# Optimization experiments

Hardware: AMD Instinct MI355X
Metric: run time of the kernel (lower is better)

The kernel has to match this reference:

```python
import jax, jax.numpy as jnp
import numpy as np
import math

B, L, DM = 2, 256, 256
H, NK, T = 8, 4, 4  # heads, num_kernels, time_dim
DH = DM // H


def _gauss_mean_over_d(t, mu, sigma, w):
    """t: [B,P,T]; mu/sigma/w: [H,D,T,K] -> mean over D of sum_{t,k} w*exp(...): [B,H,P].
    Scans over D to avoid materializing [B,H,D,P,T,K]."""
    D = mu.shape[1]

    def step(acc, p):
        mu_d, sg_d, w_d = p  # each [H,T,K]
        diff = t[:, None, :, :, None] - mu_d[None, :, None, :, :]  # [B,H,P,T,K]
        g = (w_d[None, :, None] * jnp.exp(-diff ** 2 / (2.0 * sg_d[None, :, None] ** 2))).sum((-1, -2))
        return acc + g, None

    init = jnp.zeros((t.shape[0], mu.shape[0], t.shape[1]), t.dtype)
    params = (jnp.moveaxis(mu, 1, 0), jnp.moveaxis(sigma, 1, 0), jnp.moveaxis(w, 1, 0))
    acc, _ = jax.lax.scan(jax.checkpoint(step), init, params)
    return acc / D


def setup_inputs() -> dict:
    key = jax.random.key(0)
    ks = jax.random.split(key, 16)
    s = 1.0 / math.sqrt(DM)
    return {
        "x": jax.random.normal(ks[0], (B, L, DM), jnp.float32),
        "t": jax.random.uniform(ks[1], (B, L, T), jnp.float32),
        "WQ": jax.random.normal(ks[2], (DM, DM), jnp.float32) * s,
        "WK": jax.random.normal(ks[3], (DM, DM), jnp.float32) * s,
        "WV": jax.random.normal(ks[4], (DM, DM), jnp.float32) * s,
        "WO": jax.random.normal(ks[5], (DM, DM), jnp.float32) * s,
        "bO": jnp.zeros((DM,), jnp.float32),
        "mu_abs": jax.random.normal(ks[6], (H, DH, T, NK), jnp.float32),
        "sigma_abs": jnp.abs(jax.random.normal(ks[7], (H, DH, T, NK), jnp.float32)) + 1e-5,
        "w_abs": jax.random.normal(ks[8], (H, DH, T, NK), jnp.float32),
        "mu_rel": jax.random.normal(ks[9], (H, DH, T, NK), jnp.float32),
        "sigma_rel": jnp.abs(jax.random.normal(ks[10], (H, DH, T, NK), jnp.float32)) + 1e-5,
        "w_rel": jax.random.normal(ks[11], (H, DH, T, NK), jnp.float32),
        "alpha": jnp.ones((H,), jnp.float32),
        "beta": jnp.ones((H,), jnp.float32),
        "gamma": jnp.zeros((H,), jnp.float32),
    }


def reference(x, t, WQ, WK, WV, WO, bO, mu_abs, sigma_abs, w_abs,
              mu_rel, sigma_rel, w_rel, alpha, beta, gamma):
    b, l, dm = x.shape
    h = alpha.shape[0]
    dh = dm // h

    def heads(y):  # [B,L,DM] -> [B,H,L,DH]
        return y.reshape(b, l, h, dh).transpose(0, 2, 1, 3)

    Q = heads(x @ WQ.T)
    K = heads(x @ WK.T)
    V = heads(x @ WV.T)
    Xh = heads(x)

    Pij = jnp.einsum('bhid,bhjd->bhij', Xh, Xh)

    g_abs = _gauss_mean_over_d(t, mu_abs, sigma_abs, w_abs)  # [B,H,L]
    t_rel = jnp.abs(t[:, :, None, :] - t[:, None, :, :]).reshape(b, l * l, t.shape[-1])
    g_rel = _gauss_mean_over_d(t_rel, mu_rel, sigma_rel, w_rel).reshape(b, h, l, l)

    gi = g_abs[:, :, :, None]  # [B,H,L,1]
    a = alpha[None, :, None, None]
    bb = beta[None, :, None, None]
    c = gamma[None, :, None, None]
    # original: g_abs_j = g_abs_i broadcast over j, so (g_i + g_j) == 2*gi broadcast
    A = a * Pij * (gi + gi) + bb * Pij * g_rel + c

    scores = jnp.einsum('bhid,bhjd->bhij', Q, K) / math.sqrt(dh)
    attn = jax.nn.softmax(scores * A, axis=-1)  # dropout = identity (eval)
    out = jnp.einsum('bhij,bhjd->bhid', attn, V)
    out = out.transpose(0, 2, 1, 3).reshape(b, l, dm)
    return out @ WO.T + bO
```

## Files before the change

### kernel.cpp

```cpp
#include <hip/hip_runtime.h>
#include <math.h>

constexpr int Bc = 2, Lc = 256, DMc = 256, Hc = 8, DHc = 32;
constexpr float LOG2E = 1.4426950408889634f;
constexpr float RSQRT_DH = 0.17677669529663687f;
#define EXP2 __builtin_amdgcn_exp2f

constexpr int   NTAB = 512;
constexpr float SIG0 = 0.02f;

__device__ __forceinline__ float mixsum(const float4* __restrict__ prm, float x) {
    float acc = 0.f;
    #pragma unroll 8
    for (int q = 0; q < 128; ++q) {
        float4 p = prm[q];
        float d0 = x - p.x;
        acc = fmaf(p.z, EXP2(d0 * d0 * p.y), acc);
    }
    return acc;
}

__device__ __forceinline__ void role_tab(int bx,
    const float* __restrict__ mu, const float* __restrict__ sg, const float* __restrict__ w,
    float4* __restrict__ TAB, float4* __restrict__ NLIST, int* __restrict__ NCNT,
    float* smem)
{
    float4* prm = (float4*)smem;
    float*  fs  = smem + 512;
    int*    lcnt = (int*)(smem + 772);
    int hm = bx >> 2, chunk = bx & 3;
    int h = hm >> 2, tau = hm & 3;
    int tid = threadIdx.x;

    if (tid == 0) *lcnt = 0;
    __syncthreads();
    if (tid < 128) {
        int d = tid >> 2, k = tid & 3;
        int off = h * 512 + d * 16 + tau * 4 + k;
        float s  = sg[off];
        float mv = mu[off], wv = w[off];
        float n = -(0.5f * LOG2E) / (s * s);
        bool narrow = (s < SIG0);
        prm[tid] = make_float4(mv, n, narrow ? 0.0f : wv, 0.0f);
        if (chunk == 0 && narrow) {
            int slot = atomicAdd(lcnt, 1);
            NLIST[hm * 128 + slot] = make_float4(mv, n, wv, 0.0f);
        }
    }
    __syncthreads();
    if (chunk == 0 && tid == 0) NCNT[hm] = *lcnt;

    fs[tid] = mixsum(prm, (float)(chunk * 256 + tid) * (1.0f / 1024.0f));
    if (tid == 0)
        fs[256] = mixsum(prm, (float)(chunk * 256 + 256) * (1.0f / 1024.0f));
    __syncthreads();

    if (tid < 128) {
        float f0 = fs[tid * 2], fm = fs[tid * 2 + 1], f1 = fs[tid * 2 + 2];
        float c2 = 2.0f * (f0 + f1 - 2.0f * fm);
        float c1 = f1 - f0 - c2;
        TAB[hm * NTAB + chunk * 128 + tid] = make_float4(f0, c1, c2, 0.0f);
    }
}

__device__ __forceinline__ void role_gabs(int idx, const float* __restrict__ t,
                                          const float* __restrict__ mu, const float* __restrict__ sg,
                                          const float* __restrict__ w, float* __restrict__ gabs,
                                          float* smem) {
    int h = idx & 7, b = (idx >> 3) & 1, q = idx >> 4;
    int tid = threadIdx.x;
    {
        float2 s2 = *(const float2*)(sg + h * 512 + tid * 2);
        float2 o;
        o.x = -(0.5f * LOG2E) / (s2.x * s2.x);
        o.y = -(0.5f * LOG2E) / (s2.y * s2.y);
        *(float2*)(smem + tid * 2) = o;
    }
    __syncthreads();
    int lane = tid & 63, tg = tid >> 6;
    int i = q * 64 + lane;
    float tv = t[(b * Lc + i) * 4 + tg];
    const float* muB = mu + h * 512 + tg * 4;
    const float* wB  = w  + h * 512 + tg * 4;
    const float* nsB = smem + tg * 4;
    float acc = 0.f;
    #pragma unroll 4
    for (int d = 0; d < 32; ++d) {
        float4 m4 = *(const float4*)(muB + d * 16);
        float4 w4 = *(const float4*)(wB  + d * 16);
        float4 n4 = *(const float4*)(nsB + d * 16);
        float d0 = tv - m4.x; acc = fmaf(w4.x, EXP2(d0 * d0 * n4.x), acc);
        float d1 = tv - m4.y; acc = fmaf(w4.y, EXP2(d1 * d1 * n4.y), acc);
        float d2 = tv - m4.z; acc = fmaf(w4.z, EXP2(d2 * d2 * n4.z), acc);
        float d3 = tv - m4.w; acc = fmaf(w4.w, EXP2(d3 * d3 * n4.w), acc);
    }
    float* red = smem + 512;
    __syncthreads();
    red[tg * 64 + lane] = acc;
    __syncthreads();
    if (tid < 64)
        gabs[(b * Hc + h) * Lc + q * 64 + lane] =
            (red[lane] + red[64 + lane] + red[128 + lane] + red[192 + lane]) * (1.0f / 32.0f);
}

template<int R>
__device__ __forceinline__ void stage_tile2(const float* __restrict__ src, int ld,
                                            int row0, int k0, float* __restrict__ dst, int tid) {
    int row = tid >> 3;
    int cb = (tid & 7) * 2;
    float2 v = *(const float2*)(src + (size_t)(row0 + row) * ld + k0 + cb);
    dst[(cb + 0) * (R + 1) + row] = v.x;
    dst[(cb + 1) * (R + 1) + row] = v.y;
}

__device__ __forceinline__ void gemm32(const float* __restrict__ A, const float* __restrict__ W,
                                       float* __restrict__ C, const float* __restrict__ bias,
                                       float sc, int m0, int n0, float* smem) {
    float* As = smem;
    float* Ws = smem + 16 * 33;
    int tid = threadIdx.x;
    int tx = tid & 15, ty = tid >> 4;
    float acc[2][2] = {};
    for (int k0 = 0; k0 < 256; k0 += 16) {
        stage_tile2<32>(A, 256, m0, k0, As, tid);
        stage_tile2<32>(W, 256, n0, k0, Ws, tid);
        __syncthreads();
        #pragma unroll
        for (int k = 0; k < 16; ++k) {
            float a0 = As[k * 33 + ty * 2], a1 = As[k * 33 + ty * 2 + 1];
            float w0 = Ws[k * 33 + tx * 2], w1 = Ws[k * 33 + tx * 2 + 1];
            acc[0][0] = fmaf(a0, w0, acc[0][0]);
            acc[0][1] = fmaf(a0, w1, acc[0][1]);
            acc[1][0] = fmaf(a1, w0, acc[1][0]);
            acc[1][1] = fmaf(a1, w1, acc[1][1]);
        }
        __syncthreads();
    }
    #pragma unroll
    for (int u = 0; u < 2; ++u) {
        int m = m0 + ty * 2 + u;
        #pragma unroll
        for (int v = 0; v < 2; ++v) {
            float o = acc[u][v] * sc;
            if (bias) o += bias[n0 + tx * 2 + v];
            C[(size_t)m * DMc + n0 + tx * 2 + v] = o;
        }
    }
}

__global__ void __launch_bounds__(256) k_pre(
    const float* __restrict__ x, const float* __restrict__ t,
    const float* __restrict__ WQ, const float* __restrict__ WK, const float* __restrict__ WV,
    const float* __restrict__ mu_a, const float* __restrict__ sg_a, const float* __restrict__ w_a,
    const float* __restrict__ mu_r, const float* __restrict__ sg_r, const float* __restrict__ w_r,
    float* __restrict__ Qb, float* __restrict__ Kb, float* __restrict__ Vb,
    float* __restrict__ GA,
    float4* __restrict__ TAB, float4* __restrict__ NLIST, int* __restrict__ NCNT)
{
    __shared__ __align__(16) float smem[1056];
    int bx = blockIdx.x;
    if (bx < 128) {
        role_tab(bx, mu_r, sg_r, w_r, TAB, NLIST, NCNT, smem);
    } else if (bx < 192) {
        role_gabs(bx - 128, t, mu_a, sg_a, w_a, GA, smem);
    } else {
        int idx = bx - 192;
        int z = idx >> 7;
        int r = idx & 127;
        int m0 = (r >> 3) * 32, n0 = (r & 7) * 32;
        const float* W = (z == 0) ? WQ : (z == 1) ? WK : WV;
        float* C = (z == 0) ? Qb : (z == 1) ? Kb : Vb;
        gemm32(x, W, C, nullptr, (z == 0) ? RSQRT_DH : 1.0f, m0, n0, smem);
    }
}

__global__ void __launch_bounds__(512) k_att(
    const float* __restrict__ Q, const float* __restrict__ K, const float* __restrict__ x,
    const float* __restrict__ t, const float* __restrict__ gabs,
    const float4* __restrict__ TAB, const float4* __restrict__ NLIST,
    const int* __restrict__ NCNT,
    const float* __restrict__ alpha, const float* __restrict__ beta, const float* __restrict__ gamma,
    const float* __restrict__ V, float* __restrict__ AO)
{
    __shared__ __align__(16) float sm[22224];
    float* sK  = sm;
    float* sXj = sm + 8704;
    float* sQ  = sm + 17408;
    float* sP  = sm + 18048;
    float* sRS = sm + 22208;

    int it = blockIdx.x, bh = blockIdx.y;
    int b = bh >> 3, h = bh & 7;
    int i0 = it * 16;
    int tid = threadIdx.x;

    {
        int r = tid >> 3, c4 = (tid & 7) * 4;
        #pragma unroll
        for (int u = 0; u < 4; ++u) {
            int j = r + u * 64;
            float4 kv = *(const float4*)(K + ((size_t)(b * Lc + j) * DMc + h * DHc + c4));
            float4 xj = *(const float4*)(x + ((size_t)(b * Lc + j) * DMc + h * DHc + c4));
            const float* k_ = (const float*)&kv; const float* x_ = (const float*)&xj;
            #pragma unroll
            for (int q = 0; q < 4; ++q) {
                sK [(c4 + q) * 264 + j] = k_[q];
                sXj[(c4 + q) * 264 + j] = x_[q];
            }
        }
        int i = tid >> 5, k = tid & 31;
        sQ[k * 20 + i] = Q[((size_t)(b * Lc + i0 + i) * DMc + h * DHc + k)];
    }
    __syncthreads();

    int tx = tid & 63, ty = tid >> 6;
    int i2 = ty * 2, j4 = tx * 4;
    float accS[2][4] = {}, accP[2][4] = {};
    #pragma unroll 4
    for (int k = 0; k < 32; ++k) {
        float2 qa = *(const float2*)(sQ  + k * 20  + i2);
        float2 xa = *(const float2*)(sXj + k * 264 + i0 + i2);
        float4 kb = *(const float4*)(sK  + k * 264 + j4);
        float4 xb = *(const float4*)(sXj + k * 264 + j4);
        const float* qa_ = (const float*)&qa; const float* kb_ = (const float*)&kb;
        const float* xa_ = (const float*)&xa; const float* xb_ = (const float*)&xb;
        #pragma unroll
        for (int u = 0; u < 2; ++u)
            #pragma unroll
            for (int v = 0; v < 4; ++v) {
                accS[u][v] = fmaf(qa_[u], kb_[v], accS[u][v]);
                accP[u][v] = fmaf(xa_[u], xb_[v], accP[u][v]);
            }
    }
    __syncthreads();

    {
        int jr = tid >> 3, c4 = (tid & 7) * 4;
        #pragma unroll
        for (int u = 0; u < 4; ++u) {
            int j = jr + u * 64;
            *(float4*)(sK + j * 34 + c4) =
                *(const float4*)(V + ((size_t)(b * Lc + j) * DMc + h * DHc + c4));
        }
        float4* tab = (float4*)sXj;
        const float4* src = TAB + (size_t)h * 4 * NTAB;
        #pragma unroll
        for (int u = 0; u < 4; ++u)
            tab[tid + u * 512] = src[tid + u * 512];
    }
    __syncthreads();

    float4* tab = (float4*)sXj;
    float4 tiv[2], tjv[4];
    #pragma unroll
    for (int u = 0; u < 2; ++u)
        tiv[u] = *(const float4*)(t + (size_t)(b * Lc + i0 + i2 + u) * 4);
    #pragma unroll
    for (int v = 0; v < 4; ++v)
        tjv[v] = *(const float4*)(t + (size_t)(b * Lc + j4 + v) * 4);

    float g8[2][4] = {};
    #pragma unroll
    for (int tg = 0; tg < 4; ++tg) {
        float xv[2][4];
        #pragma unroll
        for (int u = 0; u < 2; ++u) {
            float tiu = ((const float*)&tiv[u])[tg];
            #pragma unroll
            for (int v = 0; v < 4; ++v) {
                float xx = fabsf(tiu - ((const float*)&tjv[v])[tg]);
                xv[u][v] = xx;
                float xs = xx * (float)NTAB;
                int iu = min((int)xs, NTAB - 1);
                float uu = xs - (float)iu;
                float4 c = tab[tg * NTAB + iu];
                g8[u][v] += fmaf(uu, fmaf(uu, c.z, c.y), c.x);
            }
        }
        int cn = NCNT[h * 4 + tg];
        for (int nn = 0; nn < cn; ++nn) {
            float4 q = NLIST[(h * 4 + tg) * 128 + nn];
            #pragma unroll
            for (int u = 0; u < 2; ++u)
                #pragma unroll
                for (int v = 0; v < 4; ++v) {
                    float d0 = xv[u][v] - q.x;
                    g8[u][v] = fmaf(q.z, EXP2(d0 * d0 * q.y), g8[u][v]);
                }
        }
    }

    float la = alpha[h], lb = beta[h], lg = gamma[h];
    constexpr float SC = 1.0f / 32.0f;
    #pragma unroll
    for (int u = 0; u < 2; ++u) {
        float gi2 = 2.0f * la * gabs[bh * Lc + i0 + i2 + u];
        float l0 = accS[u][0] * fmaf(accP[u][0], fmaf(lb, g8[u][0] * SC, gi2), lg);
        float l1 = accS[u][1] * fmaf(accP[u][1], fmaf(lb, g8[u][1] * SC, gi2), lg);
        float l2 = accS[u][2] * fmaf(accP[u][2], fmaf(lb, g8[u][2] * SC, gi2), lg);
        float l3 = accS[u][3] * fmaf(accP[u][3], fmaf(lb, g8[u][3] * SC, gi2), lg);
        float m = fmaxf(fmaxf(l0, l1), fmaxf(l2, l3));
        #pragma unroll
        for (int s = 1; s < 64; s <<= 1) m = fmaxf(m, __shfl_xor(m, s, 64));
        float4 e;
        e.x = EXP2((l0 - m) * LOG2E); e.y = EXP2((l1 - m) * LOG2E);
        e.z = EXP2((l2 - m) * LOG2E); e.w = EXP2((l3 - m) * LOG2E);
        float su = (e.x + e.y) + (e.z + e.w);
        #pragma unroll
        for (int s = 1; s < 64; s <<= 1) su += __shfl_xor(su, s, 64);
        *(float4*)(sP + (i2 + u) * 260 + j4) = e;
        if (tx == 0) sRS[i2 + u] = 1.0f / su;
    }
    __syncthreads();

    {
        int i = tid >> 5, d = tid & 31;
        float rs = sRS[i];
        float o0 = 0.f;
        #pragma unroll 4
        for (int jj = 0; jj < 256; jj += 4) {
            float4 p4 = *(const float4*)(sP + i * 260 + jj);
            o0 = fmaf(p4.x, sK[(jj + 0) * 34 + d], o0);
            o0 = fmaf(p4.y, sK[(jj + 1) * 34 + d], o0);
            o0 = fmaf(p4.z, sK[(jj + 2) * 34 + d], o0);
            o0 = fmaf(p4.w, sK[(jj + 3) * 34 + d], o0);
        }
        AO[((size_t)(b * Lc + i0 + i) * DMc + h * DHc + d)] = o0 * rs;
    }
}

__global__ void __launch_bounds__(256) k_out(const float* __restrict__ A,
                                             const float* __restrict__ W,
                                             const float* __restrict__ bias,
                                             float* __restrict__ C) {
    __shared__ __align__(16) float smem[1056];
    gemm32(A, W, C, bias, 1.0f, blockIdx.x * 32, blockIdx.y * 32, smem);
}

extern "C" void kernel_launch(void* const* d_in, const int* in_sizes, int n_in,
                              void* d_out, int out_size, void* d_ws, size_t ws_size,
                              hipStream_t stream) {
    (void)in_sizes; (void)n_in; (void)out_size; (void)ws_size;
    const float* x      = (const float*)d_in[0];
    const float* t      = (const float*)d_in[1];
    const float* WQ     = (const float*)d_in[2];
    const float* WK     = (const float*)d_in[3];
    const float* WV     = (const float*)d_in[4];
    const float* WO     = (const float*)d_in[5];
    const float* bO     = (const float*)d_in[6];
    const float* mu_abs = (const float*)d_in[7];
    const float* sg_abs = (const float*)d_in[8];
    const float* w_abs  = (const float*)d_in[9];
    const float* mu_rel = (const float*)d_in[10];
    const float* sg_rel = (const float*)d_in[11];
    const float* w_rel  = (const float*)d_in[12];
    const float* alpha  = (const float*)d_in[13];
    const float* beta   = (const float*)d_in[14];
    const float* gamma  = (const float*)d_in[15];
    float* out = (float*)d_out;
    float* ws = (float*)d_ws;

    float* Qb = ws;
    float* Kb = ws + 131072;
    float* Vb = ws + 262144;
    float* AO = ws + 393216;
    float* GA = ws + 524288;
    float4* TAB   = (float4*)(ws + 1576960);
    float4* NLIST = (float4*)(ws + 1642496);
    int*    NCNT  = (int*)   (ws + 1658880);

    k_pre<<<dim3(576), dim3(256), 0, stream>>>(x, t, WQ, WK, WV,
                                               mu_abs, sg_abs, w_abs,
                                               mu_rel, sg_rel, w_rel,
                                               Qb, Kb, Vb, GA, TAB, NLIST, NCNT);
    k_att<<<dim3(16, 16), dim3(512), 0, stream>>>(Qb, Kb, x, t, GA,
                                                  TAB, NLIST, NCNT,
                                                  alpha, beta, gamma, Vb, AO);
    k_out<<<dim3(16, 8), dim3(256), 0, stream>>>(AO, WO, bO, out);
}
```

Baseline: 124.6 us.

## Prefetch V and spline table into registers early, split table into SoA arrays

The V tile and the relative-time spline table are now loaded into registers at kernel start and stored to dedicated shared-memory regions after the QK/XX matmul. This hides global latency behind compute and removes one barrier. The table is stored as three separate float arrays instead of float4 records. The PV product now has each thread handle two output columns over half the keys, combined with a shuffle. The cost is more shared memory per block (about 146 KB) and more registers held live across the matmul, which may reduce occupancy.

Measured after the change: 127.0 us. About the same (+1.9%).

```diff
diff --git a/kernel.cpp b/kernel.cpp
--- a/kernel.cpp
+++ b/kernel.cpp
@@ -22,7 +22,7 @@
 
 __device__ __forceinline__ void role_tab(int bx,
     const float* __restrict__ mu, const float* __restrict__ sg, const float* __restrict__ w,
-    float4* __restrict__ TAB, float4* __restrict__ NLIST, int* __restrict__ NCNT,
+    float* __restrict__ TABf, float4* __restrict__ NLIST, int* __restrict__ NCNT,
     float* smem)
 {
     float4* prm = (float4*)smem;
@@ -59,7 +59,10 @@
         float f0 = fs[tid * 2], fm = fs[tid * 2 + 1], f1 = fs[tid * 2 + 2];
         float c2 = 2.0f * (f0 + f1 - 2.0f * fm);
         float c1 = f1 - f0 - c2;
-        TAB[hm * NTAB + chunk * 128 + tid] = make_float4(f0, c1, c2, 0.0f);
+        int o = hm * NTAB + chunk * 128 + tid;
+        TABf[o]         = f0;
+        TABf[16384 + o] = c1;
+        TABf[32768 + o] = c2;
     }
 }
 
@@ -155,12 +158,12 @@
     const float* __restrict__ mu_r, const float* __restrict__ sg_r, const float* __restrict__ w_r,
     float* __restrict__ Qb, float* __restrict__ Kb, float* __restrict__ Vb,
     float* __restrict__ GA,
-    float4* __restrict__ TAB, float4* __restrict__ NLIST, int* __restrict__ NCNT)
+    float* __restrict__ TABf, float4* __restrict__ NLIST, int* __restrict__ NCNT)
 {
     __shared__ __align__(16) float smem[1056];
     int bx = blockIdx.x;
     if (bx < 128) {
-        role_tab(bx, mu_r, sg_r, w_r, TAB, NLIST, NCNT, smem);
+        role_tab(bx, mu_r, sg_r, w_r, TABf, NLIST, NCNT, smem);
     } else if (bx < 192) {
         role_gabs(bx - 128, t, mu_a, sg_a, w_a, GA, smem);
     } else {
@@ -177,23 +180,27 @@
 __global__ void __launch_bounds__(512) k_att(
     const float* __restrict__ Q, const float* __restrict__ K, const float* __restrict__ x,
     const float* __restrict__ t, const float* __restrict__ gabs,
-    const float4* __restrict__ TAB, const float4* __restrict__ NLIST,
+    const float* __restrict__ TABf, const float4* __restrict__ NLIST,
     const int* __restrict__ NCNT,
     const float* __restrict__ alpha, const float* __restrict__ beta, const float* __restrict__ gamma,
     const float* __restrict__ V, float* __restrict__ AO)
 {
-    __shared__ __align__(16) float sm[22224];
+    __shared__ __align__(16) float sm[36560];
     float* sK  = sm;
-    float* sXj = sm + 8704;
-    float* sQ  = sm + 17408;
-    float* sP  = sm + 18048;
-    float* sRS = sm + 22208;
+    float* sXj = sm + 8448;
+    float* sQ  = sm + 16896;
+    float* sV  = sm + 17536;
+    float* sT  = sm + 26240;
+    float* sP  = sm + 32384;
+    float* sRS = sm + 36544;
 
     int it = blockIdx.x, bh = blockIdx.y;
     int b = bh >> 3, h = bh & 7;
     int i0 = it * 16;
     int tid = threadIdx.x;
 
+    float4 vreg[4];
+    float4 treg[3];
     {
         int r = tid >> 3, c4 = (tid & 7) * 4;
         #pragma unroll
@@ -210,6 +217,14 @@
         }
         int i = tid >> 5, k = tid & 31;
         sQ[k * 20 + i] = Q[((size_t)(b * Lc + i0 + i) * DMc + h * DHc + k)];
+        #pragma unroll
+        for (int u = 0; u < 4; ++u) {
+            int j = r + u * 64;
+            vreg[u] = *(const float4*)(V + ((size_t)(b * Lc + j) * DMc + h * DHc + c4));
+        }
+        treg[0] = ((const float4*)(TABf +         (size_t)h * 2048))[tid];
+        treg[1] = ((const float4*)(TABf + 16384 + (size_t)h * 2048))[tid];
+        treg[2] = ((const float4*)(TABf + 32768 + (size_t)h * 2048))[tid];
     }
     __syncthreads();
 
@@ -232,25 +247,20 @@
                 accP[u][v] = fmaf(xa_[u], xb_[v], accP[u][v]);
             }
     }
-    __syncthreads();
 
     {
-        int jr = tid >> 3, c4 = (tid & 7) * 4;
+        int r = tid >> 3, c4 = (tid & 7) * 4;
         #pragma unroll
         for (int u = 0; u < 4; ++u) {
-            int j = jr + u * 64;
-            *(float4*)(sK + j * 34 + c4) =
-                *(const float4*)(V + ((size_t)(b * Lc + j) * DMc + h * DHc + c4));
-        }
-        float4* tab = (float4*)sXj;
-        const float4* src = TAB + (size_t)h * 4 * NTAB;
-        #pragma unroll
-        for (int u = 0; u < 4; ++u)
-            tab[tid + u * 512] = src[tid + u * 512];
-    }
-    __syncthreads();
-
-    float4* tab = (float4*)sXj;
+            int j = r + u * 64;
+            *(float4*)(sV + j * 34 + c4) = vreg[u];
+        }
+        ((float4*)sT)[tid]          = treg[0];
+        ((float4*)(sT + 2048))[tid] = treg[1];
+        ((float4*)(sT + 4096))[tid] = treg[2];
+    }
+    __syncthreads();
+
     float4 tiv[2], tjv[4];
     #pragma unroll
     for (int u = 0; u < 2; ++u)
@@ -273,8 +283,11 @@
                 float xs = xx * (float)NTAB;
                 int iu = min((int)xs, NTAB - 1);
                 float uu = xs - (float)iu;
-                float4 c = tab[tg * NTAB + iu];
-                g8[u][v] += fmaf(uu, fmaf(uu, c.z, c.y), c.x);
+                int base = tg * NTAB + iu;
+                float c0 = sT[base];
+                float c1 = sT[2048 + base];
+                float c2 = sT[4096 + base];
+                g8[u][v] += fmaf(uu, fmaf(uu, c2, c1), c0);
             }
         }
         int cn = NCNT[h * 4 + tg];
@@ -314,18 +327,29 @@
     __syncthreads();
 
     {
-        int i = tid >> 5, d = tid & 31;
-        float rs = sRS[i];
-        float o0 = 0.f;
+        int i = tid >> 5, dp = (tid >> 1) & 15, jh = tid & 1;
+        int d2 = dp * 2;
+        int jbase = jh * 128;
+        float o0 = 0.f, o1 = 0.f;
         #pragma unroll 4
-        for (int jj = 0; jj < 256; jj += 4) {
-            float4 p4 = *(const float4*)(sP + i * 260 + jj);
-            o0 = fmaf(p4.x, sK[(jj + 0) * 34 + d], o0);
-            o0 = fmaf(p4.y, sK[(jj + 1) * 34 + d], o0);
-            o0 = fmaf(p4.z, sK[(jj + 2) * 34 + d], o0);
-            o0 = fmaf(p4.w, sK[(jj + 3) * 34 + d], o0);
-        }
-        AO[((size_t)(b * Lc + i0 + i) * DMc + h * DHc + d)] = o0 * rs;
+        for (int jj = 0; jj < 128; jj += 4) {
+            float4 p4 = *(const float4*)(sP + i * 260 + jbase + jj);
+            float2 v0 = *(const float2*)(sV + (size_t)(jbase + jj + 0) * 34 + d2);
+            float2 v1 = *(const float2*)(sV + (size_t)(jbase + jj + 1) * 34 + d2);
+            float2 v2 = *(const float2*)(sV + (size_t)(jbase + jj + 2) * 34 + d2);
+            float2 v3 = *(const float2*)(sV + (size_t)(jbase + jj + 3) * 34 + d2);
+            o0 = fmaf(p4.x, v0.x, o0); o1 = fmaf(p4.x, v0.y, o1);
+            o0 = fmaf(p4.y, v1.x, o0); o1 = fmaf(p4.y, v1.y, o1);
+            o0 = fmaf(p4.z, v2.x, o0); o1 = fmaf(p4.z, v2.y, o1);
+            o0 = fmaf(p4.w, v3.x, o0); o1 = fmaf(p4.w, v3.y, o1);
+        }
+        o0 += __shfl_xor(o0, 1, 64);
+        o1 += __shfl_xor(o1, 1, 64);
+        if (jh == 0) {
+            float rs = sRS[i];
+            *(float2*)(AO + ((size_t)(b * Lc + i0 + i) * DMc + h * DHc + d2)) =
+                make_float2(o0 * rs, o1 * rs);
+        }
     }
 }
 
@@ -365,16 +389,16 @@
     float* Vb = ws + 262144;
     float* AO = ws + 393216;
     float* GA = ws + 524288;
-    float4* TAB   = (float4*)(ws + 1576960);
+    float* TABf   = ws + 1576960;
     float4* NLIST = (float4*)(ws + 1642496);
     int*    NCNT  = (int*)   (ws + 1658880);
 
     k_pre<<<dim3(576), dim3(256), 0, stream>>>(x, t, WQ, WK, WV,
                                                mu_abs, sg_abs, w_abs,
                                                mu_rel, sg_rel, w_rel,
-                                               Qb, Kb, Vb, GA, TAB, NLIST, NCNT);
+                                               Qb, Kb, Vb, GA, TABf, NLIST, NCNT);
     k_att<<<dim3(16, 16), dim3(512), 0, stream>>>(Qb, Kb, x, t, GA,
-                                                  TAB, NLIST, NCNT,
+                                                  TABf, NLIST, NCNT,
                                                   alpha, beta, gamma, Vb, AO);
     k_out<<<dim3(16, 8), dim3(256), 0, stream>>>(AO, WO, bO, out);
 }
```
